# Kernel tuning notes

Hardware: AMD Instinct MI355X
Metric: run time of the kernel (lower is better)

Reference implementation:

```python
import jax, jax.numpy as jnp
import numpy as np

DIM = 96
HEADS = 8
HH = 128
WW = 128
L = HH * WW
K = 256
B = 2


def setup_inputs() -> dict:
    key = jax.random.key(0)
    ks = jax.random.split(key, 8)
    s = 0.02
    return {
        "x": jax.random.normal(ks[0], (B, L, DIM), jnp.float32),
        "Wqkv": jax.random.normal(ks[1], (DIM, 3 * DIM), jnp.float32) * s,
        "W0": jax.random.normal(ks[2], (DIM, DIM), jnp.float32) * s,
        "E": jax.random.normal(ks[3], (L, K), jnp.float32) * s,
        "conv0_w": jax.random.normal(ks[4], (DIM, 1, 5, 5), jnp.float32) * s,
        "conv0_b": jnp.zeros((DIM,), jnp.float32),
        "conv_sp_w": jax.random.normal(ks[5], (DIM, 1, 7, 7), jnp.float32) * s,
        "conv_sp_b": jnp.zeros((DIM,), jnp.float32),
        "conv1_w": jax.random.normal(ks[6], (DIM, DIM, 1, 1), jnp.float32) * s,
        "conv1_b": jnp.zeros((DIM,), jnp.float32),
        "H": HH,
        "W": WW,
    }


def _conv(x, w, b, pad, dil, groups):
    y = jax.lax.conv_general_dilated(
        x, w, window_strides=(1, 1), padding=[(pad, pad), (pad, pad)],
        rhs_dilation=(dil, dil),
        dimension_numbers=("NCHW", "OIHW", "NCHW"),
        feature_group_count=groups)
    return y + b[None, :, None, None]


def _cnn_atten(x, H, W, conv0_w, conv0_b, conv_sp_w, conv_sp_b, conv1_w, conv1_b):
    # VAN-style Large-Kernel-Attention: dw5x5 -> dw7x7(dil=3) -> 1x1, gate by identity
    Bx, Lx, C = x.shape
    xi = x.reshape(Bx, H, W, C).transpose(0, 3, 1, 2)  # B,C,H,W
    a = _conv(xi, conv0_w, conv0_b, 2, 1, C)
    a = _conv(a, conv_sp_w, conv_sp_b, 9, 3, C)
    a = _conv(a, conv1_w, conv1_b, 0, 1, 1)
    out = xi * a
    return out.transpose(0, 2, 3, 1).reshape(Bx, Lx, C)


def reference(x, Wqkv, W0, E, conv0_w, conv0_b, conv_sp_w, conv_sp_b, conv1_w, conv1_b, H, W):
    Bx, Lx, C = x.shape
    dh = C // HEADS
    scale = dh ** (-0.5)
    qkv = (x @ Wqkv).reshape(Bx, Lx, 3, HEADS, dh).transpose(2, 0, 3, 1, 4)  # 3,B,h,L,d
    q, k, v = qkv[0], qkv[1], qkv[2]
    ca = _cnn_atten(x, H, W, conv0_w, conv0_b, conv_sp_w, conv_sp_b, conv1_w, conv1_b)  # B,L,C
    vf = v.transpose(0, 2, 1, 3).reshape(Bx, Lx, C)
    vf = ca * vf  # elementwise CNN gating of V
    v = vf.reshape(Bx, Lx, HEADS, dh).transpose(0, 2, 1, 3)  # B,h,L,d
    # Linformer-style sequence reduction: L -> K
    v = jnp.einsum("bhjd,jk->bhkd", v, E)
    k = jnp.einsum("bhjd,jk->bhkd", k, E)
    attn = jax.nn.softmax(jnp.einsum("bhid,bhkd->bhik", q, k) * scale, axis=-1)  # B,h,L,K
    o = jnp.einsum("bhik,bhkd->bhid", attn, v)
    o = o.transpose(0, 2, 1, 3).reshape(Bx, Lx, C)
    return o @ W0
```

## Files before the change

### kernel.cpp

```cpp
#include <hip/hip_runtime.h>

#define HH_ 128
#define WW_ 128
#define LL_ (HH_*WW_)
#define NH 8
#define DHD 12
#define KD 256
#define BB_ 2
#define NROW (BB_*LL_)

typedef __attribute__((ext_vector_type(8))) short short8v;
typedef __attribute__((ext_vector_type(4))) float f32x4;
typedef unsigned short ushortT;

__device__ __forceinline__ float4 ld4(const float* p) {
    return *reinterpret_cast<const float4*>(p);
}
__device__ __forceinline__ unsigned int pk2(float a, float b) {
    unsigned int ua = __float_as_uint(a);
    unsigned int ub = __float_as_uint(b);
    ua = (ua + 0x7FFFu + ((ua >> 16) & 1u)) >> 16;
    ub = (ub + 0x7FFFu + ((ub >> 16) & 1u)) >> 16;
    return ua | (ub << 16);
}
__device__ __forceinline__ ushortT bf1(float a) {
    unsigned int u = __float_as_uint(a);
    return (ushortT)((u + 0x7FFFu + ((u >> 16) & 1u)) >> 16);
}
__device__ __forceinline__ float ubf(ushortT v) {
    return __uint_as_float(((unsigned int)v) << 16);
}
__device__ __forceinline__ unsigned int cvtpk(float a, float b) {
    unsigned int r;
    asm("v_cvt_pk_bf16_f32 %0, %1, %2" : "=v"(r) : "v"(a), "v"(b));
    return r;
}

__global__ __launch_bounds__(256) void k_prep(const float* __restrict__ E,
        const float* __restrict__ Wq, const float* __restrict__ W0,
        const float* __restrict__ w1, ushortT* __restrict__ ET,
        ushortT* __restrict__ wqT, ushortT* __restrict__ w0T,
        ushortT* __restrict__ w1c) {
    __shared__ ushortT Tz[64*66];
    const int tid = threadIdx.x;
    if (blockIdx.x < 1024) {
        const int jt = blockIdx.x >> 2, kt = blockIdx.x & 3;
        const int j0 = jt * 64, kk0 = kt * 64;
        for (int i = tid; i < 64*16; i += 256) {
            int row = i >> 4, s4 = (i & 15) << 2;
            float4 e4 = ld4(&E[(long)(j0 + row)*256 + kk0 + s4]);
            Tz[(s4 + 0)*66 + row] = bf1(e4.x);
            Tz[(s4 + 1)*66 + row] = bf1(e4.y);
            Tz[(s4 + 2)*66 + row] = bf1(e4.z);
            Tz[(s4 + 3)*66 + row] = bf1(e4.w);
        }
        __syncthreads();
        unsigned int* Tu = (unsigned int*)Tz;
        for (int i = tid; i < 64*32; i += 256) {
            int kk = i >> 5, s = i & 31;
            ((unsigned int*)ET)[(((long)(kk0 + kk) << 14) + j0 >> 1) + s] = Tu[kk*33 + s];
        }
    } else {
        int i = (blockIdx.x - 1024)*256 + tid;
        if (i < 27648) {
            int n = i / 96, k = i % 96;
            wqT[n*96 + k] = bf1(Wq[k*288 + n]);
        } else if (i < 36864) {
            int j = i - 27648;
            int n = j / 96, k = j % 96;
            w0T[n*96 + k] = bf1(W0[k*96 + n]);
        } else if (i < 46080) {
            int j = i - 36864;
            w1c[j] = bf1(w1[j]);
        }
    }
}

__global__ __launch_bounds__(256) void k_qkv(const float* __restrict__ x,
        const ushortT* __restrict__ wqT, ushortT* __restrict__ qkv16) {
    __shared__ ushortT xb[64*104];
    const int tid = threadIdx.x;
    const int r0w = blockIdx.x * 64;
    for (int i = tid; i < 64*48; i += 256) {
        int r = i / 48, cp = i % 48;
        const float* sp = x + (long)(r0w + r)*96 + cp*2;
        ((unsigned int*)xb)[r*52 + cp] = pk2(sp[0], sp[1]);
    }
    __syncthreads();
    const int lane = tid & 63, wv = tid >> 6;
    const int l15 = lane & 15, l4 = lane >> 4;
    short8v bx[3];
#pragma unroll
    for (int kt = 0; kt < 3; ++kt)
        bx[kt] = *(const short8v*)((const short*)xb + (wv*16 + l15)*104 + kt*32 + l4*8);
#pragma unroll 2
    for (int mt = 0; mt < 18; ++mt) {
        f32x4 acc = {0.f, 0.f, 0.f, 0.f};
#pragma unroll
        for (int kt = 0; kt < 3; ++kt) {
            short8v a = *(const short8v*)((const short*)wqT + (mt*16 + l15)*96 + kt*32 + l4*8);
            acc = __builtin_amdgcn_mfma_f32_16x16x32_bf16(a, bx[kt], acc, 0, 0, 0);
        }
        unsigned int* q32 = (unsigned int*)(qkv16 + (long)(r0w + wv*16 + l15)*288 + mt*16 + l4*4);
        q32[0] = pk2(acc[0], acc[1]);
        q32[1] = pk2(acc[2], acc[3]);
    }
}

__global__ __launch_bounds__(256) void k_dw5(const float* __restrict__ xin,
                                             const float* __restrict__ w,
                                             const float* __restrict__ bias,
                                             float* __restrict__ out) {
    __shared__ float wl[25][96];
    const int tid = threadIdx.x;
    for (int i = tid; i < 25*96; i += 256) {
        int c = i / 25, t = i % 25;
        wl[t][c] = w[i];
    }
    __syncthreads();
    const int c4 = (tid & 7)*4;
    const int px = tid >> 3;
    const int pix0 = blockIdx.x * 32;
    const int b = pix0 >> 14;
    const int y = (pix0 & 16383) >> 7;
    const int xx = (pix0 & 127) + px;
    float4 acc[3];
#pragma unroll
    for (int ch = 0; ch < 3; ++ch) { acc[ch].x=0.f; acc[ch].y=0.f; acc[ch].z=0.f; acc[ch].w=0.f; }
#pragma unroll
    for (int iy = 0; iy < 5; ++iy) {
        int y2 = y + iy - 2;
        if (y2 < 0 || y2 >= HH_) continue;
#pragma unroll
        for (int ix = 0; ix < 5; ++ix) {
            int x2 = xx + ix - 2;
            if (x2 < 0 || x2 >= WW_) continue;
            const float* src = xin + ((b << 14) + y2*WW_ + x2)*96;
            const float* wt = &wl[iy*5 + ix][0];
#pragma unroll
            for (int ch = 0; ch < 3; ++ch) {
                float4 xv = ld4(src + ch*32 + c4);
                float4 wv = ld4(wt + ch*32 + c4);
                acc[ch].x = fmaf(xv.x, wv.x, acc[ch].x);
                acc[ch].y = fmaf(xv.y, wv.y, acc[ch].y);
                acc[ch].z = fmaf(xv.z, wv.z, acc[ch].z);
                acc[ch].w = fmaf(xv.w, wv.w, acc[ch].w);
            }
        }
    }
    float* dst = out + (long)(pix0 + px)*96;
#pragma unroll
    for (int ch = 0; ch < 3; ++ch) {
        float4 bv = ld4(bias + ch*32 + c4);
        float4 r;
        r.x = acc[ch].x + bv.x; r.y = acc[ch].y + bv.y;
        r.z = acc[ch].z + bv.z; r.w = acc[ch].w + bv.w;
        *reinterpret_cast<float4*>(dst + ch*32 + c4) = r;
    }
}

__global__ __launch_bounds__(256) void k_dw7(const float* __restrict__ xin,
                                             const float* __restrict__ w,
                                             const float* __restrict__ bias,
                                             float* __restrict__ out) {
    __shared__ float wl[49][96];
    const int tid = threadIdx.x;
    for (int i = tid; i < 49*96; i += 256) {
        int c = i / 49, t = i % 49;
        wl[t][c] = w[i];
    }
    __syncthreads();
    const int c4 = (tid & 7)*4;
    const int px = tid >> 3;
    const int pix0 = blockIdx.x * 32;
    const int b = pix0 >> 14;
    const int y = (pix0 & 16383) >> 7;
    const int xx = (pix0 & 127) + px;
    float4 acc[3];
#pragma unroll
    for (int ch = 0; ch < 3; ++ch) { acc[ch].x=0.f; acc[ch].y=0.f; acc[ch].z=0.f; acc[ch].w=0.f; }
#pragma unroll
    for (int iy = 0; iy < 7; ++iy) {
        int y2 = y + iy*3 - 9;
        if (y2 < 0 || y2 >= HH_) continue;
#pragma unroll
        for (int ix = 0; ix < 7; ++ix) {
            int x2 = xx + ix*3 - 9;
            if (x2 < 0 || x2 >= WW_) continue;
            const float* src = xin + ((b << 14) + y2*WW_ + x2)*96;
            const float* wt = &wl[iy*7 + ix][0];
#pragma unroll
            for (int ch = 0; ch < 3; ++ch) {
                float4 xv = ld4(src + ch*32 + c4);
                float4 wv = ld4(wt + ch*32 + c4);
                acc[ch].x = fmaf(xv.x, wv.x, acc[ch].x);
                acc[ch].y = fmaf(xv.y, wv.y, acc[ch].y);
                acc[ch].z = fmaf(xv.z, wv.z, acc[ch].z);
                acc[ch].w = fmaf(xv.w, wv.w, acc[ch].w);
            }
        }
    }
    float* dst = out + (long)(pix0 + px)*96;
#pragma unroll
    for (int ch = 0; ch < 3; ++ch) {
        float4 bv = ld4(bias + ch*32 + c4);
        float4 r;
        r.x = acc[ch].x + bv.x; r.y = acc[ch].y + bv.y;
        r.z = acc[ch].z + bv.z; r.w = acc[ch].w + bv.w;
        *reinterpret_cast<float4*>(dst + ch*32 + c4) = r;
    }
}

__global__ __launch_bounds__(256) void k_pw_gate(const float* __restrict__ a2,
        const ushortT* __restrict__ w1c, const float* __restrict__ b1,
        const float* __restrict__ xin, const ushortT* __restrict__ qkv16,
        ushortT* __restrict__ XT) {
    __shared__ ushortT ab[64*104];
    __shared__ ushortT ktile[96*66];
    __shared__ ushortT vtile[96*66];
    const int tid = threadIdx.x;
    const int r0 = blockIdx.x * 64;
    const int b = r0 >> 14, j0 = r0 & 16383;
    for (int i = tid; i < 64*48; i += 256) {
        int r = i / 48, cp = i % 48;
        const float* sp = a2 + (long)(r0 + r)*96 + cp*2;
        ((unsigned int*)ab)[r*52 + cp] = pk2(sp[0], sp[1]);
    }
    const unsigned int* q32 = (const unsigned int*)qkv16;
    for (int i = tid; i < 64*48; i += 256) {
        int row = i / 48, cp = i % 48;
        unsigned int kk2 = q32[(long)(r0 + row)*144 + 48 + cp];
        ktile[(2*cp + 0)*66 + row] = (ushortT)(kk2 & 0xFFFF);
        ktile[(2*cp + 1)*66 + row] = (ushortT)(kk2 >> 16);
    }
    __syncthreads();
    const int lane = tid & 63, wv = tid >> 6;
    const int l15 = lane & 15, l4 = lane >> 4;
    const int row = r0 + wv*16 + l15;
    const int jloc = wv*16 + l15;
    short8v bx[3];
#pragma unroll
    for (int kt = 0; kt < 3; ++kt)
        bx[kt] = *(const short8v*)((const short*)ab + (wv*16 + l15)*104 + kt*32 + l4*8);
#pragma unroll
    for (int mt = 0; mt < 6; ++mt) {
        f32x4 acc = {0.f, 0.f, 0.f, 0.f};
#pragma unroll
        for (int kt = 0; kt < 3; ++kt) {
            short8v a = *(const short8v*)((const short*)w1c + (mt*16 + l15)*96 + kt*32 + l4*8);
            acc = __builtin_amdgcn_mfma_f32_16x16x32_bf16(a, bx[kt], acc, 0, 0, 0);
        }
        const int c0 = mt*16 + l4*4;
        float4 b4 = ld4(&b1[c0]);
        float4 x4 = ld4(&xin[(long)row*96 + c0]);
        uint2 vv = *reinterpret_cast<const uint2*>(qkv16 + (long)row*288 + 192 + c0);
        float v0 = ubf((ushortT)(vv.x & 0xFFFF)), v1 = ubf((ushortT)(vv.x >> 16));
        float v2 = ubf((ushortT)(vv.y & 0xFFFF)), v3 = ubf((ushortT)(vv.y >> 16));
        vtile[(c0 + 0)*66 + jloc] = bf1(x4.x * v0 * (acc[0] + b4.x));
        vtile[(c0 + 1)*66 + jloc] = bf1(x4.y * v1 * (acc[1] + b4.y));
        vtile[(c0 + 2)*66 + jloc] = bf1(x4.z * v2 * (acc[2] + b4.z));
        vtile[(c0 + 3)*66 + jloc] = bf1(x4.w * v3 * (acc[3] + b4.w));
    }
    __syncthreads();
    unsigned int* XTu = (unsigned int*)XT;
    unsigned int* ku = (unsigned int*)ktile;
    unsigned int* vu = (unsigned int*)vtile;
    for (int i = tid; i < 96*32; i += 256) {
        int cc = i >> 5, s = i & 31;
        XTu[((((long)b*192 + cc) << 14) + j0 >> 1) + s] = ku[cc*33 + s];
    }
    for (int i = tid; i < 96*32; i += 256) {
        int cc = i >> 5, s = i & 31;
        XTu[((((long)b*192 + 96 + cc) << 14) + j0 >> 1) + s] = vu[cc*33 + s];
    }
}

__global__ __launch_bounds__(512, 2) void k_ered(const ushortT* __restrict__ ET,
        const ushortT* __restrict__ XT, ushortT* __restrict__ part16) {
    const int tid = threadIdx.x;
    const int lane = tid & 63, wv = tid >> 6;
    const int l15 = lane & 15, l4 = lane >> 4;
    const int mtg = wv & 3, nth = wv >> 2;
    const int b  = blockIdx.x >> 7;
    const int jc = blockIdx.x & 127;
    const int j0 = jc * 128;
    f32x4 acc[4][6];
#pragma unroll
    for (int mi = 0; mi < 4; ++mi)
#pragma unroll
        for (int ni = 0; ni < 6; ++ni)
            acc[mi][ni] = (f32x4){0.f, 0.f, 0.f, 0.f};
    const ushortT* Ab = ET + ((long)(mtg*64 + l15) << 14) + j0 + l4*8;
    const ushortT* Bb = XT + (((long)b*192 + nth*96 + l15) << 14) + j0 + l4*8;
#pragma unroll
    for (int ks = 0; ks < 4; ++ks) {
        short8v a[4], bx[6];
#pragma unroll
        for (int mi = 0; mi < 4; ++mi)
            a[mi] = *(const short8v*)(Ab + ((long)mi << 18) + ks*32);
#pragma unroll
        for (int ni = 0; ni < 6; ++ni)
            bx[ni] = *(const short8v*)(Bb + ((long)ni << 18) + ks*32);
#pragma unroll
        for (int mi = 0; mi < 4; ++mi)
#pragma unroll
            for (int ni = 0; ni < 6; ++ni)
                acc[mi][ni] = __builtin_amdgcn_mfma_f32_16x16x32_bf16(a[mi], bx[ni], acc[mi][ni], 0, 0, 0);
    }
    const long base = (long)(b*128 + jc)*49152;
#pragma unroll
    for (int mi = 0; mi < 4; ++mi) {
        int kkb = (mtg*4 + mi)*16 + l4*4;
#pragma unroll
        for (int ni = 0; ni < 6; ++ni) {
            int cc = (nth*6 + ni)*16 + l15;
#pragma unroll
            for (int r = 0; r < 4; ++r)
                part16[base + (long)(kkb + r)*192 + cc] = bf1(acc[mi][ni][r]);
        }
    }
}

__global__ __launch_bounds__(256) void k_ered_fin(const ushortT* __restrict__ part16,
        ushortT* __restrict__ kp16, ushortT* __restrict__ vp16) {
    const int idx = blockIdx.x*256 + threadIdx.x;
    const int c  = idx % 96;
    const int kk = (idx / 96) % 256;
    const int m  = (idx / (96*256)) % 2;
    const int b  = idx / (96*256*2);
    float s = 0.f;
    long off = ((long)(b*128)*256 + kk)*192 + m*96 + c;
    for (int jc = 0; jc < 128; ++jc) {
        s += ubf(part16[off]);
        off += 49152;
    }
    const int h = c / DHD, d = c % DHD;
    if (m == 0) {
        kp16[((b*NH + h)*256 + kk)*16 + d] = bf1(s * 0.4164701998f);
        if (d < 4) kp16[((b*NH + h)*256 + kk)*16 + 12 + d] = 0;
    } else {
        vp16[((b*NH + h)*16 + d)*256 + kk] = bf1(s);
        if (d < 4)
            vp16[((b*NH + h)*16 + 12 + d)*256 + kk] = (d == 0) ? (ushortT)0x3F80 : (ushortT)0;
    }
}

__global__ __launch_bounds__(256, 4) void k_attn(const ushortT* __restrict__ qkv16,
        const ushortT* __restrict__ kp16, const ushortT* __restrict__ vp16,
        ushortT* __restrict__ obuf) {
    __shared__ ushortT lds[24720];
    const int tid = threadIdx.x;
    const int lane = tid & 63, wv = tid >> 6;
    const int l15 = lane & 15, l4 = lane >> 4;
    const int bid = blockIdx.x;
    const int r0 = (bid >> 3) * 64;
    const int h = bid & 7;
    const int b = r0 >> 14;
    {
        const uint4* ksrc = (const uint4*)(kp16 + ((long)(b*NH + h) << 12));
        uint4* kdst = (uint4*)lds;
        kdst[tid] = ksrc[tid];
        kdst[256 + tid] = ksrc[256 + tid];
        const uint4* vsrc = (const uint4*)(vp16 + ((long)(b*NH + h) << 12));
        uint4* vdst = (uint4*)(lds + 4112);
        int r1 = tid >> 5, s1 = tid & 31;
        vdst[r1*33 + s1] = vsrc[tid];
        int j2 = tid + 256;
        int r2 = j2 >> 5, s2 = j2 & 31;
        vdst[r2*33 + s2] = vsrc[j2];
        if (tid < 2) ((uint4*)(lds + 4096))[tid] = (uint4){0u, 0u, 0u, 0u};
    }
    __syncthreads();
    ushortT* Pw = lds + 8336 + wv*4096;
    unsigned int* Pu = (unsigned int*)Pw;
    const int wbase = (l4 >> 1)*64 + l15*4 + (l4 & 1)*2;
    const f32x4 z = {0.f, 0.f, 0.f, 0.f};
    const int row0 = r0 + wv*16;
    short8v bq = {0, 0, 0, 0, 0, 0, 0, 0};
    {
        unsigned int* bq32 = (unsigned int*)&bq;
        const ushortT* qp = qkv16 + (long)(row0 + l15)*288 + h*12;
        if (l4 == 0) {
            uint2 t0 = *reinterpret_cast<const uint2*>(qp);
            uint2 t1 = *reinterpret_cast<const uint2*>(qp + 4);
            bq32[0] = t0.x; bq32[1] = t0.y; bq32[2] = t1.x; bq32[3] = t1.y;
        } else if (l4 == 1) {
            uint2 t0 = *reinterpret_cast<const uint2*>(qp + 8);
            bq32[0] = t0.x; bq32[1] = t0.y;
        }
    }
    const ushortT* kpl = lds + l15*16 + l4*8;
#pragma unroll
    for (int mt = 0; mt < 16; ++mt) {
        short8v a = *(const short8v*)(kpl + mt*256);
        f32x4 s = __builtin_amdgcn_mfma_f32_16x16x32_bf16(a, bq, z, 0, 0, 0);
        unsigned int* dst = Pu + (mt >> 1)*256 + (mt & 1)*128 + wbase;
        dst[0] = cvtpk(exp2f(s[0]), exp2f(s[1]));
        dst[1] = cvtpk(exp2f(s[2]), exp2f(s[3]));
    }
    f32x4 o = z;
    const ushortT* vpl = lds + 4112 + l15*264 + l4*8;
#pragma unroll
    for (int ks = 0; ks < 8; ++ks) {
        short8v bp = *(const short8v*)(Pw + ks*512 + l4*128 + l15*8);
        short8v av = *(const short8v*)(vpl + ks*32);
        o = __builtin_amdgcn_mfma_f32_16x16x32_bf16(av, bp, o, 0, 0, 0);
    }
    float rinv = 1.0f / __shfl(o[0], 48 + l15, 64);
    if (l4 < 3) {
        unsigned int* od = (unsigned int*)(obuf + (long)(row0 + l15)*96 + h*12 + l4*4);
        od[0] = cvtpk(o[0]*rinv, o[1]*rinv);
        od[1] = cvtpk(o[2]*rinv, o[3]*rinv);
    }
}

__global__ __launch_bounds__(256) void k_out(const ushortT* __restrict__ obuf,
        const ushortT* __restrict__ w0T, float* __restrict__ out) {
    __shared__ ushortT ol[64*104];
    const int tid = threadIdx.x;
    const int r0 = blockIdx.x * 64;
    for (int i = tid; i < 768; i += 256) {
        int r = i / 12, sg = i % 12;
        *reinterpret_cast<uint4*>(&ol[r*104 + sg*8]) =
            *reinterpret_cast<const uint4*>(&obuf[(long)(r0 + r)*96 + sg*8]);
    }
    __syncthreads();
    const int lane = tid & 63, wv = tid >> 6;
    const int l15 = lane & 15, l4 = lane >> 4;
    short8v a[3];
#pragma unroll
    for (int kt = 0; kt < 3; ++kt)
        a[kt] = *(const short8v*)((const short*)ol + (wv*16 + l15)*104 + kt*32 + l4*8);
#pragma unroll
    for (int nt = 0; nt < 6; ++nt) {
        f32x4 acc = {0.f, 0.f, 0.f, 0.f};
#pragma unroll
        for (int kt = 0; kt < 3; ++kt) {
            short8v bw = *(const short8v*)((const short*)w0T + (nt*16 + l15)*96 + kt*32 + l4*8);
            acc = __builtin_amdgcn_mfma_f32_16x16x32_bf16(a[kt], bw, acc, 0, 0, 0);
        }
#pragma unroll
        for (int r = 0; r < 4; ++r)
            out[(long)(r0 + wv*16 + l4*4 + r)*96 + nt*16 + l15] = acc[r];
    }
}

extern "C" void kernel_launch(void* const* d_in, const int* in_sizes, int n_in,
                              void* d_out, int out_size, void* d_ws, size_t ws_size,
                              hipStream_t stream) {
    (void)in_sizes; (void)n_in; (void)out_size; (void)ws_size;
    const float* x    = (const float*)d_in[0];
    const float* Wqkv = (const float*)d_in[1];
    const float* W0   = (const float*)d_in[2];
    const float* E    = (const float*)d_in[3];
    const float* c0w  = (const float*)d_in[4];
    const float* c0b  = (const float*)d_in[5];
    const float* cspw = (const float*)d_in[6];
    const float* cspb = (const float*)d_in[7];
    const float* c1w  = (const float*)d_in[8];
    const float* c1b  = (const float*)d_in[9];
    float* out = (float*)d_out;
    float* ws  = (float*)d_ws;

    ushortT* qkv16  = (ushortT*)ws;
    ushortT* wqT16  = (ushortT*)(ws + 4718592);
    ushortT* w0T16  = (ushortT*)(ws + 4732416);
    ushortT* w1c16  = (ushortT*)(ws + 4737024);
    ushortT* ET16   = (ushortT*)(ws + 4741632);
    ushortT* XT16   = (ushortT*)(ws + 6838784);
    float* a1   = ws + 9984512;
    float* a2   = ws + 13130240;
    ushortT* part16 = (ushortT*)(ws + 9984512);
    ushortT* obuf   = (ushortT*)(ws + 9984512);
    ushortT* kp16   = (ushortT*)(ws + 16275968);
    ushortT* vp16   = (ushortT*)(ws + 16308736);

    k_prep<<<dim3(1204), dim3(256), 0, stream>>>(E, Wqkv, W0, c1w, ET16, wqT16, w0T16, w1c16);
    k_qkv<<<dim3(NROW/64), dim3(256), 0, stream>>>(x, wqT16, qkv16);
    k_dw5<<<dim3(NROW/32), dim3(256), 0, stream>>>(x, c0w, c0b, a1);
    k_dw7<<<dim3(NROW/32), dim3(256), 0, stream>>>(a1, cspw, cspb, a2);
    k_pw_gate<<<dim3(NROW/64), dim3(256), 0, stream>>>(a2, w1c16, c1b, x, qkv16, XT16);
    k_ered<<<dim3(256), dim3(512), 0, stream>>>(ET16, XT16, part16);
    k_ered_fin<<<dim3(384), dim3(256), 0, stream>>>(part16, kp16, vp16);
    k_attn<<<dim3((NROW/64)*NH), dim3(256), 0, stream>>>(qkv16, kp16, vp16, obuf);
    k_out<<<dim3(NROW/64), dim3(256), 0, stream>>>(obuf, w0T16, out);
}
```

Before: 145.6 us.

## Merge independent front-end kernels horizontally and store dw7 output as bf16

The dw5 conv is folded into the weight/E prep kernel, and the QKV projection and dw7 conv now share one launch by splitting on block index. This cuts the launch count from five to three and lets independent work run concurrently. The dw7 output is written as packed bf16 instead of fp32, which halves that intermediate's write and read traffic and removes a conversion in k_pw_gate. The cost is mixed-role blocks with a larger shared allocation, and a2 rounding to bf16 now happens before the pointwise GEMM rather than inside it.

After: 132.2 us. 1.1x faster.

```diff
diff --git a/kernel.cpp b/kernel.cpp
--- a/kernel.cpp
+++ b/kernel.cpp
@@ -36,15 +36,65 @@
     return r;
 }
 
-__global__ __launch_bounds__(256) void k_prep(const float* __restrict__ E,
-        const float* __restrict__ Wq, const float* __restrict__ W0,
-        const float* __restrict__ w1, ushortT* __restrict__ ET,
+__global__ __launch_bounds__(256) void k_front(const float* __restrict__ x,
+        const float* __restrict__ c0w, const float* __restrict__ c0b,
+        const float* __restrict__ E, const float* __restrict__ Wq,
+        const float* __restrict__ W0, const float* __restrict__ w1,
+        float* __restrict__ a1, ushortT* __restrict__ ET,
         ushortT* __restrict__ wqT, ushortT* __restrict__ w0T,
         ushortT* __restrict__ w1c) {
-    __shared__ ushortT Tz[64*66];
+    __shared__ __align__(16) float shf[2400];
     const int tid = threadIdx.x;
     if (blockIdx.x < 1024) {
-        const int jt = blockIdx.x >> 2, kt = blockIdx.x & 3;
+        float* wl = shf;
+        for (int i = tid; i < 25*96; i += 256) {
+            int c = i / 25, t = i % 25;
+            wl[t*96 + c] = c0w[i];
+        }
+        __syncthreads();
+        const int c4 = (tid & 7)*4;
+        const int px = tid >> 3;
+        const int pix0 = blockIdx.x * 32;
+        const int b = pix0 >> 14;
+        const int y = (pix0 & 16383) >> 7;
+        const int xx = (pix0 & 127) + px;
+        float4 acc[3];
+#pragma unroll
+        for (int ch = 0; ch < 3; ++ch) { acc[ch].x=0.f; acc[ch].y=0.f; acc[ch].z=0.f; acc[ch].w=0.f; }
+#pragma unroll
+        for (int iy = 0; iy < 5; ++iy) {
+            int y2 = y + iy - 2;
+            if (y2 < 0 || y2 >= HH_) continue;
+#pragma unroll
+            for (int ix = 0; ix < 5; ++ix) {
+                int x2 = xx + ix - 2;
+                if (x2 < 0 || x2 >= WW_) continue;
+                const float* src = x + ((b << 14) + y2*WW_ + x2)*96;
+                const float* wt = &wl[(iy*5 + ix)*96];
+#pragma unroll
+                for (int ch = 0; ch < 3; ++ch) {
+                    float4 xv = ld4(src + ch*32 + c4);
+                    float4 wv = ld4(wt + ch*32 + c4);
+                    acc[ch].x = fmaf(xv.x, wv.x, acc[ch].x);
+                    acc[ch].y = fmaf(xv.y, wv.y, acc[ch].y);
+                    acc[ch].z = fmaf(xv.z, wv.z, acc[ch].z);
+                    acc[ch].w = fmaf(xv.w, wv.w, acc[ch].w);
+                }
+            }
+        }
+        float* dst = a1 + (long)(pix0 + px)*96;
+#pragma unroll
+        for (int ch = 0; ch < 3; ++ch) {
+            float4 bv = ld4(c0b + ch*32 + c4);
+            float4 r;
+            r.x = acc[ch].x + bv.x; r.y = acc[ch].y + bv.y;
+            r.z = acc[ch].z + bv.z; r.w = acc[ch].w + bv.w;
+            *reinterpret_cast<float4*>(dst + ch*32 + c4) = r;
+        }
+    } else if (blockIdx.x < 2048) {
+        ushortT* Tz = (ushortT*)shf;
+        const int bid = blockIdx.x - 1024;
+        const int jt = bid >> 2, kt = bid & 3;
         const int j0 = jt * 64, kk0 = kt * 64;
         for (int i = tid; i < 64*16; i += 256) {
             int row = i >> 4, s4 = (i & 15) << 2;
@@ -61,7 +111,7 @@
             ((unsigned int*)ET)[(((long)(kk0 + kk) << 14) + j0 >> 1) + s] = Tu[kk*33 + s];
         }
     } else {
-        int i = (blockIdx.x - 1024)*256 + tid;
+        int i = (blockIdx.x - 2048)*256 + tid;
         if (i < 27648) {
             int n = i / 96, k = i % 96;
             wqT[n*96 + k] = bf1(Wq[k*288 + n]);
@@ -76,142 +126,88 @@
     }
 }
 
-__global__ __launch_bounds__(256) void k_qkv(const float* __restrict__ x,
-        const ushortT* __restrict__ wqT, ushortT* __restrict__ qkv16) {
-    __shared__ ushortT xb[64*104];
-    const int tid = threadIdx.x;
-    const int r0w = blockIdx.x * 64;
-    for (int i = tid; i < 64*48; i += 256) {
-        int r = i / 48, cp = i % 48;
-        const float* sp = x + (long)(r0w + r)*96 + cp*2;
-        ((unsigned int*)xb)[r*52 + cp] = pk2(sp[0], sp[1]);
-    }
-    __syncthreads();
-    const int lane = tid & 63, wv = tid >> 6;
-    const int l15 = lane & 15, l4 = lane >> 4;
-    short8v bx[3];
-#pragma unroll
-    for (int kt = 0; kt < 3; ++kt)
-        bx[kt] = *(const short8v*)((const short*)xb + (wv*16 + l15)*104 + kt*32 + l4*8);
+__global__ __launch_bounds__(256) void k_mid(const float* __restrict__ x,
+        const ushortT* __restrict__ wqT, ushortT* __restrict__ qkv16,
+        const float* __restrict__ a1, const float* __restrict__ cspw,
+        const float* __restrict__ cspb, ushortT* __restrict__ a2_16) {
+    __shared__ __align__(16) float shm[4704];
+    const int tid = threadIdx.x;
+    if (blockIdx.x < 512) {
+        ushortT* xb = (ushortT*)shm;
+        const int r0w = blockIdx.x * 64;
+        for (int i = tid; i < 64*48; i += 256) {
+            int r = i / 48, cp = i % 48;
+            const float* sp = x + (long)(r0w + r)*96 + cp*2;
+            ((unsigned int*)xb)[r*52 + cp] = pk2(sp[0], sp[1]);
+        }
+        __syncthreads();
+        const int lane = tid & 63, wv = tid >> 6;
+        const int l15 = lane & 15, l4 = lane >> 4;
+        short8v bx[3];
+#pragma unroll
+        for (int kt = 0; kt < 3; ++kt)
+            bx[kt] = *(const short8v*)((const short*)xb + (wv*16 + l15)*104 + kt*32 + l4*8);
 #pragma unroll 2
-    for (int mt = 0; mt < 18; ++mt) {
-        f32x4 acc = {0.f, 0.f, 0.f, 0.f};
-#pragma unroll
-        for (int kt = 0; kt < 3; ++kt) {
-            short8v a = *(const short8v*)((const short*)wqT + (mt*16 + l15)*96 + kt*32 + l4*8);
-            acc = __builtin_amdgcn_mfma_f32_16x16x32_bf16(a, bx[kt], acc, 0, 0, 0);
-        }
-        unsigned int* q32 = (unsigned int*)(qkv16 + (long)(r0w + wv*16 + l15)*288 + mt*16 + l4*4);
-        q32[0] = pk2(acc[0], acc[1]);
-        q32[1] = pk2(acc[2], acc[3]);
-    }
-}
-
-__global__ __launch_bounds__(256) void k_dw5(const float* __restrict__ xin,
-                                             const float* __restrict__ w,
-                                             const float* __restrict__ bias,
-                                             float* __restrict__ out) {
-    __shared__ float wl[25][96];
-    const int tid = threadIdx.x;
-    for (int i = tid; i < 25*96; i += 256) {
-        int c = i / 25, t = i % 25;
-        wl[t][c] = w[i];
-    }
-    __syncthreads();
-    const int c4 = (tid & 7)*4;
-    const int px = tid >> 3;
-    const int pix0 = blockIdx.x * 32;
-    const int b = pix0 >> 14;
-    const int y = (pix0 & 16383) >> 7;
-    const int xx = (pix0 & 127) + px;
-    float4 acc[3];
-#pragma unroll
-    for (int ch = 0; ch < 3; ++ch) { acc[ch].x=0.f; acc[ch].y=0.f; acc[ch].z=0.f; acc[ch].w=0.f; }
-#pragma unroll
-    for (int iy = 0; iy < 5; ++iy) {
-        int y2 = y + iy - 2;
-        if (y2 < 0 || y2 >= HH_) continue;
-#pragma unroll
-        for (int ix = 0; ix < 5; ++ix) {
-            int x2 = xx + ix - 2;
-            if (x2 < 0 || x2 >= WW_) continue;
-            const float* src = xin + ((b << 14) + y2*WW_ + x2)*96;
-            const float* wt = &wl[iy*5 + ix][0];
-#pragma unroll
-            for (int ch = 0; ch < 3; ++ch) {
-                float4 xv = ld4(src + ch*32 + c4);
-                float4 wv = ld4(wt + ch*32 + c4);
-                acc[ch].x = fmaf(xv.x, wv.x, acc[ch].x);
-                acc[ch].y = fmaf(xv.y, wv.y, acc[ch].y);
-                acc[ch].z = fmaf(xv.z, wv.z, acc[ch].z);
-                acc[ch].w = fmaf(xv.w, wv.w, acc[ch].w);
+        for (int mt = 0; mt < 18; ++mt) {
+            f32x4 acc = {0.f, 0.f, 0.f, 0.f};
+#pragma unroll
+            for (int kt = 0; kt < 3; ++kt) {
+                short8v a = *(const short8v*)((const short*)wqT + (mt*16 + l15)*96 + kt*32 + l4*8);
+                acc = __builtin_amdgcn_mfma_f32_16x16x32_bf16(a, bx[kt], acc, 0, 0, 0);
             }
-        }
-    }
-    float* dst = out + (long)(pix0 + px)*96;
-#pragma unroll
-    for (int ch = 0; ch < 3; ++ch) {
-        float4 bv = ld4(bias + ch*32 + c4);
-        float4 r;
-        r.x = acc[ch].x + bv.x; r.y = acc[ch].y + bv.y;
-        r.z = acc[ch].z + bv.z; r.w = acc[ch].w + bv.w;
-        *reinterpret_cast<float4*>(dst + ch*32 + c4) = r;
-    }
-}
-
-__global__ __launch_bounds__(256) void k_dw7(const float* __restrict__ xin,
-                                             const float* __restrict__ w,
-                                             const float* __restrict__ bias,
-                                             float* __restrict__ out) {
-    __shared__ float wl[49][96];
-    const int tid = threadIdx.x;
-    for (int i = tid; i < 49*96; i += 256) {
-        int c = i / 49, t = i % 49;
-        wl[t][c] = w[i];
-    }
-    __syncthreads();
-    const int c4 = (tid & 7)*4;
-    const int px = tid >> 3;
-    const int pix0 = blockIdx.x * 32;
-    const int b = pix0 >> 14;
-    const int y = (pix0 & 16383) >> 7;
-    const int xx = (pix0 & 127) + px;
-    float4 acc[3];
-#pragma unroll
-    for (int ch = 0; ch < 3; ++ch) { acc[ch].x=0.f; acc[ch].y=0.f; acc[ch].z=0.f; acc[ch].w=0.f; }
-#pragma unroll
-    for (int iy = 0; iy < 7; ++iy) {
-        int y2 = y + iy*3 - 9;
-        if (y2 < 0 || y2 >= HH_) continue;
-#pragma unroll
-        for (int ix = 0; ix < 7; ++ix) {
-            int x2 = xx + ix*3 - 9;
-            if (x2 < 0 || x2 >= WW_) continue;
-            const float* src = xin + ((b << 14) + y2*WW_ + x2)*96;
-            const float* wt = &wl[iy*7 + ix][0];
-#pragma unroll
-            for (int ch = 0; ch < 3; ++ch) {
-                float4 xv = ld4(src + ch*32 + c4);
-                float4 wv = ld4(wt + ch*32 + c4);
-                acc[ch].x = fmaf(xv.x, wv.x, acc[ch].x);
-                acc[ch].y = fmaf(xv.y, wv.y, acc[ch].y);
-                acc[ch].z = fmaf(xv.z, wv.z, acc[ch].z);
-                acc[ch].w = fmaf(xv.w, wv.w, acc[ch].w);
+            unsigned int* q32 = (unsigned int*)(qkv16 + (long)(r0w + wv*16 + l15)*288 + mt*16 + l4*4);
+            q32[0] = pk2(acc[0], acc[1]);
+            q32[1] = pk2(acc[2], acc[3]);
+        }
+    } else {
+        float* wl = shm;
+        for (int i = tid; i < 49*96; i += 256) {
+            int c = i / 49, t = i % 49;
+            wl[t*96 + c] = cspw[i];
+        }
+        __syncthreads();
+        const int c4 = (tid & 7)*4;
+        const int px = tid >> 3;
+        const int pix0 = (blockIdx.x - 512) * 32;
+        const int b = pix0 >> 14;
+        const int y = (pix0 & 16383) >> 7;
+        const int xx = (pix0 & 127) + px;
+        float4 acc[3];
+#pragma unroll
+        for (int ch = 0; ch < 3; ++ch) { acc[ch].x=0.f; acc[ch].y=0.f; acc[ch].z=0.f; acc[ch].w=0.f; }
+#pragma unroll
+        for (int iy = 0; iy < 7; ++iy) {
+            int y2 = y + iy*3 - 9;
+            if (y2 < 0 || y2 >= HH_) continue;
+#pragma unroll
+            for (int ix = 0; ix < 7; ++ix) {
+                int x2 = xx + ix*3 - 9;
+                if (x2 < 0 || x2 >= WW_) continue;
+                const float* src = a1 + ((b << 14) + y2*WW_ + x2)*96;
+                const float* wt = &wl[(iy*7 + ix)*96];
+#pragma unroll
+                for (int ch = 0; ch < 3; ++ch) {
+                    float4 xv = ld4(src + ch*32 + c4);
+                    float4 wv = ld4(wt + ch*32 + c4);
+                    acc[ch].x = fmaf(xv.x, wv.x, acc[ch].x);
+                    acc[ch].y = fmaf(xv.y, wv.y, acc[ch].y);
+                    acc[ch].z = fmaf(xv.z, wv.z, acc[ch].z);
+                    acc[ch].w = fmaf(xv.w, wv.w, acc[ch].w);
+                }
             }
         }
-    }
-    float* dst = out + (long)(pix0 + px)*96;
-#pragma unroll
-    for (int ch = 0; ch < 3; ++ch) {
-        float4 bv = ld4(bias + ch*32 + c4);
-        float4 r;
-        r.x = acc[ch].x + bv.x; r.y = acc[ch].y + bv.y;
-        r.z = acc[ch].z + bv.z; r.w = acc[ch].w + bv.w;
-        *reinterpret_cast<float4*>(dst + ch*32 + c4) = r;
-    }
-}
-
-__global__ __launch_bounds__(256) void k_pw_gate(const float* __restrict__ a2,
+        ushortT* dst = a2_16 + (long)(pix0 + px)*96;
+#pragma unroll
+        for (int ch = 0; ch < 3; ++ch) {
+            float4 bv = ld4(cspb + ch*32 + c4);
+            unsigned int* d32 = (unsigned int*)(dst + ch*32 + c4);
+            d32[0] = pk2(acc[ch].x + bv.x, acc[ch].y + bv.y);
+            d32[1] = pk2(acc[ch].z + bv.z, acc[ch].w + bv.w);
+        }
+    }
+}
+
+__global__ __launch_bounds__(256) void k_pw_gate(const ushortT* __restrict__ a2_16,
         const ushortT* __restrict__ w1c, const float* __restrict__ b1,
         const float* __restrict__ xin, const ushortT* __restrict__ qkv16,
         ushortT* __restrict__ XT) {
@@ -221,10 +217,10 @@
     const int tid = threadIdx.x;
     const int r0 = blockIdx.x * 64;
     const int b = r0 >> 14, j0 = r0 & 16383;
+    const unsigned int* a2u = (const unsigned int*)a2_16;
     for (int i = tid; i < 64*48; i += 256) {
         int r = i / 48, cp = i % 48;
-        const float* sp = a2 + (long)(r0 + r)*96 + cp*2;
-        ((unsigned int*)ab)[r*52 + cp] = pk2(sp[0], sp[1]);
+        ((unsigned int*)ab)[r*52 + cp] = a2u[(long)(r0 + r)*48 + cp];
     }
     const unsigned int* q32 = (const unsigned int*)qkv16;
     for (int i = tid; i < 64*48; i += 256) {
@@ -468,18 +464,17 @@
     ushortT* w1c16  = (ushortT*)(ws + 4737024);
     ushortT* ET16   = (ushortT*)(ws + 4741632);
     ushortT* XT16   = (ushortT*)(ws + 6838784);
-    float* a1   = ws + 9984512;
-    float* a2   = ws + 13130240;
+    float* a1       = ws + 9984512;
+    ushortT* a2_16  = (ushortT*)(ws + 13130240);
     ushortT* part16 = (ushortT*)(ws + 9984512);
     ushortT* obuf   = (ushortT*)(ws + 9984512);
     ushortT* kp16   = (ushortT*)(ws + 16275968);
     ushortT* vp16   = (ushortT*)(ws + 16308736);
 
-    k_prep<<<dim3(1204), dim3(256), 0, stream>>>(E, Wqkv, W0, c1w, ET16, wqT16, w0T16, w1c16);
-    k_qkv<<<dim3(NROW/64), dim3(256), 0, stream>>>(x, wqT16, qkv16);
-    k_dw5<<<dim3(NROW/32), dim3(256), 0, stream>>>(x, c0w, c0b, a1);
-    k_dw7<<<dim3(NROW/32), dim3(256), 0, stream>>>(a1, cspw, cspb, a2);
-    k_pw_gate<<<dim3(NROW/64), dim3(256), 0, stream>>>(a2, w1c16, c1b, x, qkv16, XT16);
+    k_front<<<dim3(2228), dim3(256), 0, stream>>>(x, c0w, c0b, E, Wqkv, W0, c1w,
+                                                  a1, ET16, wqT16, w0T16, w1c16);
+    k_mid<<<dim3(1536), dim3(256), 0, stream>>>(x, wqT16, qkv16, a1, cspw, cspb, a2_16);
+    k_pw_gate<<<dim3(NROW/64), dim3(256), 0, stream>>>(a2_16, w1c16, c1b, x, qkv16, XT16);
     k_ered<<<dim3(256), dim3(512), 0, stream>>>(ET16, XT16, part16);
     k_ered_fin<<<dim3(384), dim3(256), 0, stream>>>(part16, kp16, vp16);
     k_attn<<<dim3((NROW/64)*NH), dim3(256), 0, stream>>>(qkv16, kp16, vp16, obuf);
```
